# Performance work log

Measured on AMD Instinct MI355X. Metric: run time of the kernel, lower is better.

The kernel has to match this reference:

```python
import jax, jax.numpy as jnp
import numpy as np

N_NODES = 100000
N_EDGES = 1600000
D_IN = 128
D_HID = 128
GARMENT_SIZE = 80000


def setup_inputs() -> dict:
    key = jax.random.key(0)
    k1, k2, k3, k4, k5, k6 = jax.random.split(key, 6)
    notes = jax.random.normal(k1, (N_NODES, D_IN), dtype=jnp.float32)
    w = jax.random.normal(k2, (D_IN, D_HID), dtype=jnp.float32) * 0.05
    b = jax.random.normal(k3, (D_HID,), dtype=jnp.float32) * 0.05
    edge_src = jax.random.randint(k4, (N_EDGES,), 0, N_NODES, dtype=jnp.int32)
    edge_dst = jax.random.randint(k5, (N_EDGES,), 0, N_NODES, dtype=jnp.int32)
    edge_w = jax.random.uniform(k6, (N_EDGES,), dtype=jnp.float32)
    return {
        "notes": notes,
        "w": w,
        "b": b,
        "edge_src": edge_src,
        "edge_dst": edge_dst,
        "edge_w": edge_w,
        "garment_size": GARMENT_SIZE,
    }


def reference(notes, w, b, edge_src, edge_dst, edge_w, garment_size):
    # Dense projection: X0 = notes @ w   -> [N, H]
    X0 = jnp.einsum("nd,dh->nh", notes, w)
    # edge_convolution_template(edge_function=lambda x, y: y, reduction='weighted'):
    # X1[i] = sum over edges (i -> j) of a_ij * X0[j]
    msgs = X0[edge_dst] * edge_w[:, None]                      # [E, H] gather + scale
    X1 = jax.ops.segment_sum(msgs, edge_src, num_segments=notes.shape[0])  # [N, H]
    X = X1 + b
    # concat(act(X), X0[garment_size:]) along node axis -> [2N - garment_size, H]
    return jnp.concatenate([jax.nn.relu(X), X0[garment_size:]], axis=0)
```

## Files before the change

### kernel.cpp

```cpp
#include <hip/hip_runtime.h>

#define H 128
#define NPB 256
#define NB_MAX 1024
#define FILL_CH 4096
#define CNT_BLOCKS 256

static __device__ __forceinline__ unsigned short f2bf(float f) {
  unsigned u = __float_as_uint(f);
  u += 0x7FFFu + ((u >> 16) & 1u);
  return (unsigned short)(u >> 16);
}

__global__ __launch_bounds__(256) void gemm_count_kernel(
    const float* __restrict__ notes, const float* __restrict__ w,
    const int* __restrict__ g_ptr, const int* __restrict__ esrc,
    unsigned short* __restrict__ x0h, float* __restrict__ out,
    int* __restrict__ bucketCount, int nb, int n_nodes, int n_edges,
    int cntBlocks) {
  __shared__ float wtile[32 * H];
  __shared__ float ntile[64 * 32];
  const int tid = threadIdx.x;

  if (blockIdx.x < cntBlocks) {
    int* cnt = (int*)wtile;
    for (int i = tid; i < nb; i += 256) cnt[i] = 0;
    __syncthreads();
    int i = blockIdx.x * 256 + tid;
    const int stride = cntBlocks * 256;
    for (; i < n_edges; i += stride) atomicAdd(&cnt[esrc[i] >> 8], 1);
    __syncthreads();
    for (int j = tid; j < nb; j += 256) {
      const int c = cnt[j];
      if (c) atomicAdd(&bucketCount[j], c);
    }
    return;
  }

  const int tx = tid & 31;
  const int ty = tid >> 5;
  const int rowBlk = (blockIdx.x - cntBlocks) * 64;
  const int g = *g_ptr;

  float acc[8][4];
#pragma unroll
  for (int i = 0; i < 8; ++i)
#pragma unroll
    for (int j = 0; j < 4; ++j) acc[i][j] = 0.f;

  for (int kc = 0; kc < H; kc += 32) {
    __syncthreads();
    {
      const float4* wg = (const float4*)(w + (size_t)kc * H);
      float4* wl = (float4*)wtile;
#pragma unroll
      for (int i = 0; i < 4; ++i) wl[tid + i * 256] = wg[tid + i * 256];
    }
    {
      float4* nl = (float4*)ntile;
#pragma unroll
      for (int i = 0; i < 2; ++i) {
        const int idx = tid + i * 256;
        const int row = idx >> 3;
        const int q = idx & 7;
        const int rr = min(rowBlk + row, n_nodes - 1);
        nl[idx] = *(const float4*)(notes + (size_t)rr * H + kc + q * 4);
      }
    }
    __syncthreads();
#pragma unroll 8
    for (int kk = 0; kk < 32; ++kk) {
      const float4 b4 = *(const float4*)&wtile[kk * H + tx * 4];
      float a[8];
#pragma unroll
      for (int i = 0; i < 8; ++i) a[i] = ntile[(ty * 8 + i) * 32 + kk];
#pragma unroll
      for (int i = 0; i < 8; ++i) {
        acc[i][0] += a[i] * b4.x;
        acc[i][1] += a[i] * b4.y;
        acc[i][2] += a[i] * b4.z;
        acc[i][3] += a[i] * b4.w;
      }
    }
  }

#pragma unroll
  for (int i = 0; i < 8; ++i) {
    const int r = rowBlk + ty * 8 + i;
    if (r < n_nodes) {
      ushort4 h;
      h.x = f2bf(acc[i][0]);
      h.y = f2bf(acc[i][1]);
      h.z = f2bf(acc[i][2]);
      h.w = f2bf(acc[i][3]);
      *(ushort4*)(x0h + (size_t)r * H + tx * 4) = h;
      if (r >= g) {
        float4 v;
        v.x = acc[i][0]; v.y = acc[i][1]; v.z = acc[i][2]; v.w = acc[i][3];
        *(float4*)(out + (size_t)(n_nodes + r - g) * H + tx * 4) = v;
      }
    }
  }
}

__global__ __launch_bounds__(256) void bucket_scan_kernel(
    const int* __restrict__ bucketCount, int* __restrict__ bucketBase,
    int* __restrict__ bucketCursor, int* __restrict__ off, int nb,
    int n_nodes, int n_edges) {
  __shared__ int part[256];
  const int t = threadIdx.x;
  const int K = (nb + 255) / 256;
  const int lo = t * K;
  const int hi = min(lo + K, nb);
  int sum = 0;
  for (int i = lo; i < hi; ++i) sum += bucketCount[i];
  part[t] = sum;
  __syncthreads();
  for (int o = 1; o < 256; o <<= 1) {
    const int tv = (t >= o) ? part[t - o] : 0;
    __syncthreads();
    part[t] += tv;
    __syncthreads();
  }
  int run = (t == 0) ? 0 : part[t - 1];
  for (int i = lo; i < hi; ++i) {
    bucketBase[i] = run;
    bucketCursor[i] = run;
    run += bucketCount[i];
  }
  if (t == 255) {
    bucketBase[nb] = part[255];
    off[n_nodes] = n_edges;
  }
}

__global__ __launch_bounds__(256) void bucket_fill_kernel(
    const int* __restrict__ esrc, const int* __restrict__ edst,
    const float* __restrict__ ew, int* __restrict__ bucketCursor,
    int2* __restrict__ sedge, unsigned char* __restrict__ srcloc, int n_edges,
    int nb) {
  __shared__ int2 stage[FILL_CH];
  __shared__ unsigned short bkt16[FILL_CH];
  __shared__ unsigned char loc8[FILL_CH];
  __shared__ int cntA[NB_MAX];
  __shared__ int lbase[NB_MAX];
  __shared__ int cntC[NB_MAX];
  const int t = threadIdx.x;
  const int base = blockIdx.x * FILL_CH;
  const int edgesInBlock = min(FILL_CH, n_edges - base);

  for (int i = t; i < nb; i += 256) {
    cntA[i] = 0;
    cntC[i] = 0;
  }
  __syncthreads();

  int sreg[FILL_CH / 256];
#pragma unroll
  for (int k = 0; k < FILL_CH / 256; ++k) {
    const int e = base + k * 256 + t;
    if (e < n_edges) {
      const int s = esrc[e];
      sreg[k] = s;
      atomicAdd(&cntA[s >> 8], 1);
    }
  }
  __syncthreads();

  {
    __shared__ int part[256];
    const int K = (nb + 255) / 256;
    const int lo = t * K;
    const int hi = min(lo + K, nb);
    int sum = 0;
    for (int i = lo; i < hi; ++i) sum += cntA[i];
    part[t] = sum;
    __syncthreads();
    for (int o = 1; o < 256; o <<= 1) {
      const int tv = (t >= o) ? part[t - o] : 0;
      __syncthreads();
      part[t] += tv;
      __syncthreads();
    }
    int run = (t == 0) ? 0 : part[t - 1];
    for (int i = lo; i < hi; ++i) {
      lbase[i] = run;
      run += cntA[i];
    }
  }
  __syncthreads();
  for (int i = t; i < nb; i += 256) {
    const int c = cntA[i];
    cntA[i] = c ? atomicAdd(&bucketCursor[i], c) : 0;
  }
  __syncthreads();

#pragma unroll
  for (int k = 0; k < FILL_CH / 256; ++k) {
    const int e = base + k * 256 + t;
    if (e < n_edges) {
      const int s = sreg[k];
      const int b = s >> 8;
      const int r = atomicAdd(&cntC[b], 1);
      const int sp = lbase[b] + r;
      int2 pk;
      pk.x = edst[e];
      pk.y = __float_as_int(ew[e]);
      stage[sp] = pk;
      bkt16[sp] = (unsigned short)b;
      loc8[sp] = (unsigned char)(s & 255);
    }
  }
  __syncthreads();

  for (int j = t; j < edgesInBlock; j += 256) {
    const int b = bkt16[j];
    const int pos = cntA[b] + (j - lbase[b]);
    sedge[pos] = stage[j];
    srcloc[pos] = loc8[j];
  }
}

__global__ __launch_bounds__(256) void bucket_sort_kernel(
    const int* __restrict__ bucketBase, const int2* __restrict__ sedge,
    const unsigned char* __restrict__ srcloc, int2* __restrict__ sedge2,
    int* __restrict__ off, int n_nodes) {
  __shared__ int cnt[NPB];
  __shared__ int nodeOff[NPB];
  const int t = threadIdx.x;
  const int beg = bucketBase[blockIdx.x];
  const int end = bucketBase[blockIdx.x + 1];
  const int nodeBase = blockIdx.x * NPB;
  const int nodesInBucket = min(NPB, n_nodes - nodeBase);

  cnt[t] = 0;
  __syncthreads();
  for (int j = beg + t; j < end; j += 256) atomicAdd(&cnt[srcloc[j]], 1);
  __syncthreads();
  {
    const int v = cnt[t];
    nodeOff[t] = v;
    __syncthreads();
    for (int o = 1; o < 256; o <<= 1) {
      const int tv = (t >= o) ? nodeOff[t - o] : 0;
      __syncthreads();
      nodeOff[t] += tv;
      __syncthreads();
    }
    nodeOff[t] -= v;
  }
  if (t < nodesInBucket) off[nodeBase + t] = beg + nodeOff[t];
  cnt[t] = 0;
  __syncthreads();
  for (int j = beg + t; j < end; j += 256) {
    const int loc = srcloc[j];
    const int r = atomicAdd(&cnt[loc], 1);
    sedge2[beg + nodeOff[loc] + r] = sedge[j];
  }
}

__global__ __launch_bounds__(256) void gather_kernel(
    const int* __restrict__ off, const int2* __restrict__ sedge,
    const unsigned short* __restrict__ x0h, const float* __restrict__ b,
    float* __restrict__ out, int n_nodes) {
  const int wave = blockIdx.x * (blockDim.x >> 6) + (threadIdx.x >> 6);
  const int lane = threadIdx.x & 63;
  const int q = lane >> 4;
  const int l16 = lane & 15;
  const int node = wave * 4 + q;
  const bool valid = (node < n_nodes);

  int begH = 0, endH = 0;
  if (valid) {
    begH = off[node];
    endH = off[node + 1];
  }
  const int degH = endH - begH;
  const int dO = __shfl_xor(degH, 16);
  int kmin = min(degH, dO);
  int kmax = max(degH, dO);
  kmin = min(kmin, __shfl_xor(kmin, 32));
  kmax = max(kmax, __shfl_xor(kmax, 32));
  const int kfull = kmin & ~3;
  const int lastH = max(endH - 1, 0);
  const int2* __restrict__ sp = sedge + begH;

  const unsigned* __restrict__ x0u = (const unsigned*)x0h;

  float4 aLo[4], aHi[4];
#pragma unroll
  for (int j = 0; j < 4; ++j) {
    aLo[j] = make_float4(0.f, 0.f, 0.f, 0.f);
    aHi[j] = make_float4(0.f, 0.f, 0.f, 0.f);
  }

  int k = 0;
  for (; k < kfull; k += 4) {
    int2 m[4];
#pragma unroll
    for (int j = 0; j < 4; ++j) m[j] = sp[k + j];
    uint4 u[4];
#pragma unroll
    for (int j = 0; j < 4; ++j)
      u[j] = *(const uint4*)(x0u + (size_t)m[j].x * 64 + l16 * 4);
#pragma unroll
    for (int j = 0; j < 4; ++j) {
      const float wv = __int_as_float(m[j].y);
      aLo[j].x += __uint_as_float(u[j].x << 16) * wv;
      aLo[j].y += __uint_as_float(u[j].x & 0xFFFF0000u) * wv;
      aLo[j].z += __uint_as_float(u[j].y << 16) * wv;
      aLo[j].w += __uint_as_float(u[j].y & 0xFFFF0000u) * wv;
      aHi[j].x += __uint_as_float(u[j].z << 16) * wv;
      aHi[j].y += __uint_as_float(u[j].z & 0xFFFF0000u) * wv;
      aHi[j].z += __uint_as_float(u[j].w << 16) * wv;
      aHi[j].w += __uint_as_float(u[j].w & 0xFFFF0000u) * wv;
    }
  }
  for (; k < kmax; k += 4) {
    int2 m[4];
#pragma unroll
    for (int j = 0; j < 4; ++j) m[j] = sedge[min(begH + k + j, lastH)];
    uint4 u[4];
#pragma unroll
    for (int j = 0; j < 4; ++j)
      u[j] = *(const uint4*)(x0u + (size_t)m[j].x * 64 + l16 * 4);
#pragma unroll
    for (int j = 0; j < 4; ++j) {
      const float wv = (k + j < degH) ? __int_as_float(m[j].y) : 0.f;
      aLo[j].x += __uint_as_float(u[j].x << 16) * wv;
      aLo[j].y += __uint_as_float(u[j].x & 0xFFFF0000u) * wv;
      aLo[j].z += __uint_as_float(u[j].y << 16) * wv;
      aLo[j].w += __uint_as_float(u[j].y & 0xFFFF0000u) * wv;
      aHi[j].x += __uint_as_float(u[j].z << 16) * wv;
      aHi[j].y += __uint_as_float(u[j].z & 0xFFFF0000u) * wv;
      aHi[j].z += __uint_as_float(u[j].w << 16) * wv;
      aHi[j].w += __uint_as_float(u[j].w & 0xFFFF0000u) * wv;
    }
  }

  const float4 b0 = ((const float4*)b)[l16 * 2];
  const float4 b1 = ((const float4*)b)[l16 * 2 + 1];
  float4 r0, r1;
  r0.x = fmaxf(aLo[0].x + aLo[1].x + aLo[2].x + aLo[3].x + b0.x, 0.f);
  r0.y = fmaxf(aLo[0].y + aLo[1].y + aLo[2].y + aLo[3].y + b0.y, 0.f);
  r0.z = fmaxf(aLo[0].z + aLo[1].z + aLo[2].z + aLo[3].z + b0.z, 0.f);
  r0.w = fmaxf(aLo[0].w + aLo[1].w + aLo[2].w + aLo[3].w + b0.w, 0.f);
  r1.x = fmaxf(aHi[0].x + aHi[1].x + aHi[2].x + aHi[3].x + b1.x, 0.f);
  r1.y = fmaxf(aHi[0].y + aHi[1].y + aHi[2].y + aHi[3].y + b1.y, 0.f);
  r1.z = fmaxf(aHi[0].z + aHi[1].z + aHi[2].z + aHi[3].z + b1.z, 0.f);
  r1.w = fmaxf(aHi[0].w + aHi[1].w + aHi[2].w + aHi[3].w + b1.w, 0.f);
  if (valid) {
    float4* o4 = (float4*)out + (size_t)node * 32 + l16 * 2;
    o4[0] = r0;
    o4[1] = r1;
  }
}

__global__ __launch_bounds__(256) void scatter_kernel(
    const int* __restrict__ esrc, const int* __restrict__ edst,
    const float* __restrict__ ew, const unsigned short* __restrict__ x0h,
    float* __restrict__ acc, int n_edges) {
  const int lane = threadIdx.x & 63;
  const int waveId = blockIdx.x * (blockDim.x >> 6) + (threadIdx.x >> 6);
  const int nWaves = gridDim.x * (blockDim.x >> 6);
  const unsigned* __restrict__ x0u = (const unsigned*)x0h;
  for (int e = waveId; e < n_edges; e += nWaves) {
    const int s = esrc[e];
    const int d = edst[e];
    const float wt = ew[e];
    const unsigned u = x0u[(size_t)d * 64 + lane];
    float* p = acc + (size_t)s * H + lane * 2;
    atomicAdd(p, __uint_as_float(u << 16) * wt);
    atomicAdd(p + 1, __uint_as_float(u & 0xFFFF0000u) * wt);
  }
}

__global__ __launch_bounds__(256) void epilogue_kernel(
    float* __restrict__ out, const float* __restrict__ b, int n4) {
  const int i = blockIdx.x * blockDim.x + threadIdx.x;
  if (i >= n4) return;
  float4* o4 = (float4*)out;
  const float4* b4 = (const float4*)b;
  float4 v = o4[i];
  const float4 bb = b4[i & 31];
  v.x = fmaxf(v.x + bb.x, 0.f);
  v.y = fmaxf(v.y + bb.y, 0.f);
  v.z = fmaxf(v.z + bb.z, 0.f);
  v.w = fmaxf(v.w + bb.w, 0.f);
  o4[i] = v;
}

extern "C" void kernel_launch(void* const* d_in, const int* in_sizes, int n_in,
                              void* d_out, int out_size, void* d_ws, size_t ws_size,
                              hipStream_t stream) {
  const float* notes = (const float*)d_in[0];
  const float* w     = (const float*)d_in[1];
  const float* b     = (const float*)d_in[2];
  const int*   esrc  = (const int*)d_in[3];
  const int*   edst  = (const int*)d_in[4];
  const float* ew    = (const float*)d_in[5];
  const int*   gptr  = (const int*)d_in[6];

  const int n_nodes = in_sizes[0] / H;
  const int n_edges = in_sizes[3];
  float* out = (float*)d_out;

  const int nb = (n_nodes + NPB - 1) / NPB;

  char* ws = (char*)d_ws;
  size_t p = 0;
  auto alloc = [&](size_t bytes) -> char* {
    char* cur = ws + p;
    p = (p + bytes + 255) & ~(size_t)255;
    return cur;
  };
  unsigned short* x0h = (unsigned short*)alloc((size_t)n_nodes * H * 2);
  int*  bucketCount  = (int*)alloc((size_t)nb * sizeof(int));
  int*  bucketBase   = (int*)alloc(((size_t)nb + 1) * sizeof(int));
  int*  bucketCursor = (int*)alloc((size_t)nb * sizeof(int));
  int*  off          = (int*)alloc(((size_t)n_nodes + 1) * sizeof(int));
  int2* sedge        = (int2*)alloc((size_t)n_edges * sizeof(int2));
  int2* sedge2       = (int2*)alloc((size_t)n_edges * sizeof(int2));
  unsigned char* srcloc = (unsigned char*)alloc((size_t)n_edges);
  const bool ok = (p <= ws_size) && (nb <= NB_MAX);

  const int gemmBlocks = (n_nodes + 63) / 64;

  if (ok) {
    hipMemsetAsync(bucketCount, 0, (size_t)nb * sizeof(int), stream);
    gemm_count_kernel<<<gemmBlocks + CNT_BLOCKS, 256, 0, stream>>>(
        notes, w, gptr, esrc, x0h, out, bucketCount, nb, n_nodes, n_edges,
        CNT_BLOCKS);
    bucket_scan_kernel<<<1, 256, 0, stream>>>(bucketCount, bucketBase,
                                              bucketCursor, off, nb, n_nodes,
                                              n_edges);
    bucket_fill_kernel<<<(n_edges + FILL_CH - 1) / FILL_CH, 256, 0, stream>>>(
        esrc, edst, ew, bucketCursor, sedge, srcloc, n_edges, nb);
    bucket_sort_kernel<<<nb, 256, 0, stream>>>(bucketBase, sedge, srcloc,
                                               sedge2, off, n_nodes);
    const int waves = (n_nodes + 3) / 4;
    gather_kernel<<<(waves + 3) / 4, 256, 0, stream>>>(off, sedge2, x0h, b,
                                                       out, n_nodes);
  } else {
    gemm_count_kernel<<<gemmBlocks, 256, 0, stream>>>(
        notes, w, gptr, esrc, x0h, out, bucketCount, 0, n_nodes, n_edges, 0);
    hipMemsetAsync(d_out, 0, (size_t)n_nodes * H * sizeof(float), stream);
    scatter_kernel<<<2048, 256, 0, stream>>>(esrc, edst, ew, x0h, out, n_edges);
    const int n4 = n_nodes * H / 4;
    epilogue_kernel<<<(n4 + 255) / 256, 256, 0, stream>>>(out, b, n4);
  }
}
```

Baseline: 271.3 us.

## Fuse per-bucket node sort with gather into one LDS-staged kernel

The second-level bucket sort and the gather are merged into one kernel. Each block now sorts its bucket's edges by source node into shared memory and then immediately runs the weighted gather for its 128 nodes, so the sorted edge array and the per-node offset array no longer make a round trip through global memory. Bucket size is halved to 128 nodes so a bucket's edges (about 2048 on average) fit in a 4096-entry LDS buffer, with a chunked fallback that accumulates partial sums in the output. The cost is fewer, heavier blocks (about 782) with many barriers, and the gather now runs at block rather than wave granularity, which may lower occupancy and parallelism.

```diff
diff --git a/kernel.cpp b/kernel.cpp
--- a/kernel.cpp
+++ b/kernel.cpp
@@ -1,10 +1,11 @@
 #include <hip/hip_runtime.h>
 
 #define H 128
-#define NPB 256
+#define NPB 128
 #define NB_MAX 1024
 #define FILL_CH 4096
 #define CNT_BLOCKS 256
+#define GCAP 4096
 
 static __device__ __forceinline__ unsigned short f2bf(float f) {
   unsigned u = __float_as_uint(f);
@@ -28,7 +29,7 @@
     __syncthreads();
     int i = blockIdx.x * 256 + tid;
     const int stride = cntBlocks * 256;
-    for (; i < n_edges; i += stride) atomicAdd(&cnt[esrc[i] >> 8], 1);
+    for (; i < n_edges; i += stride) atomicAdd(&cnt[esrc[i] >> 7], 1);
     __syncthreads();
     for (int j = tid; j < nb; j += 256) {
       const int c = cnt[j];
@@ -105,8 +106,7 @@
 
 __global__ __launch_bounds__(256) void bucket_scan_kernel(
     const int* __restrict__ bucketCount, int* __restrict__ bucketBase,
-    int* __restrict__ bucketCursor, int* __restrict__ off, int nb,
-    int n_nodes, int n_edges) {
+    int* __restrict__ bucketCursor, int nb) {
   __shared__ int part[256];
   const int t = threadIdx.x;
   const int K = (nb + 255) / 256;
@@ -128,10 +128,7 @@
     bucketCursor[i] = run;
     run += bucketCount[i];
   }
-  if (t == 255) {
-    bucketBase[nb] = part[255];
-    off[n_nodes] = n_edges;
-  }
+  if (t == 255) bucketBase[nb] = part[255];
 }
 
 __global__ __launch_bounds__(256) void bucket_fill_kernel(
@@ -162,7 +159,7 @@
     if (e < n_edges) {
       const int s = esrc[e];
       sreg[k] = s;
-      atomicAdd(&cntA[s >> 8], 1);
+      atomicAdd(&cntA[s >> 7], 1);
     }
   }
   __syncthreads();
@@ -200,7 +197,7 @@
     const int e = base + k * 256 + t;
     if (e < n_edges) {
       const int s = sreg[k];
-      const int b = s >> 8;
+      const int b = s >> 7;
       const int r = atomicAdd(&cntC[b], 1);
       const int sp = lbase[b] + r;
       int2 pk;
@@ -208,7 +205,7 @@
       pk.y = __float_as_int(ew[e]);
       stage[sp] = pk;
       bkt16[sp] = (unsigned short)b;
-      loc8[sp] = (unsigned char)(s & 255);
+      loc8[sp] = (unsigned char)(s & 127);
     }
   }
   __syncthreads();
@@ -221,138 +218,151 @@
   }
 }
 
-__global__ __launch_bounds__(256) void bucket_sort_kernel(
+__global__ __launch_bounds__(256) void sortgather_kernel(
     const int* __restrict__ bucketBase, const int2* __restrict__ sedge,
-    const unsigned char* __restrict__ srcloc, int2* __restrict__ sedge2,
-    int* __restrict__ off, int n_nodes) {
+    const unsigned char* __restrict__ srcloc,
+    const unsigned short* __restrict__ x0h, const float* __restrict__ b,
+    float* __restrict__ out, int n_nodes) {
+  __shared__ int2 ledge[GCAP];
   __shared__ int cnt[NPB];
   __shared__ int nodeOff[NPB];
   const int t = threadIdx.x;
+  const int lane = t & 63;
+  const int wv = t >> 6;
+  const int q = lane >> 4;
+  const int l16 = lane & 15;
   const int beg = bucketBase[blockIdx.x];
   const int end = bucketBase[blockIdx.x + 1];
   const int nodeBase = blockIdx.x * NPB;
-  const int nodesInBucket = min(NPB, n_nodes - nodeBase);
-
-  cnt[t] = 0;
-  __syncthreads();
-  for (int j = beg + t; j < end; j += 256) atomicAdd(&cnt[srcloc[j]], 1);
-  __syncthreads();
-  {
-    const int v = cnt[t];
-    nodeOff[t] = v;
-    __syncthreads();
-    for (int o = 1; o < 256; o <<= 1) {
-      const int tv = (t >= o) ? nodeOff[t - o] : 0;
-      __syncthreads();
-      nodeOff[t] += tv;
-      __syncthreads();
-    }
-    nodeOff[t] -= v;
-  }
-  if (t < nodesInBucket) off[nodeBase + t] = beg + nodeOff[t];
-  cnt[t] = 0;
-  __syncthreads();
-  for (int j = beg + t; j < end; j += 256) {
-    const int loc = srcloc[j];
-    const int r = atomicAdd(&cnt[loc], 1);
-    sedge2[beg + nodeOff[loc] + r] = sedge[j];
-  }
-}
-
-__global__ __launch_bounds__(256) void gather_kernel(
-    const int* __restrict__ off, const int2* __restrict__ sedge,
-    const unsigned short* __restrict__ x0h, const float* __restrict__ b,
-    float* __restrict__ out, int n_nodes) {
-  const int wave = blockIdx.x * (blockDim.x >> 6) + (threadIdx.x >> 6);
-  const int lane = threadIdx.x & 63;
-  const int q = lane >> 4;
-  const int l16 = lane & 15;
-  const int node = wave * 4 + q;
-  const bool valid = (node < n_nodes);
-
-  int begH = 0, endH = 0;
-  if (valid) {
-    begH = off[node];
-    endH = off[node + 1];
-  }
-  const int degH = endH - begH;
-  const int dO = __shfl_xor(degH, 16);
-  int kmin = min(degH, dO);
-  int kmax = max(degH, dO);
-  kmin = min(kmin, __shfl_xor(kmin, 32));
-  kmax = max(kmax, __shfl_xor(kmax, 32));
-  const int kfull = kmin & ~3;
-  const int lastH = max(endH - 1, 0);
-  const int2* __restrict__ sp = sedge + begH;
-
   const unsigned* __restrict__ x0u = (const unsigned*)x0h;
-
-  float4 aLo[4], aHi[4];
-#pragma unroll
-  for (int j = 0; j < 4; ++j) {
-    aLo[j] = make_float4(0.f, 0.f, 0.f, 0.f);
-    aHi[j] = make_float4(0.f, 0.f, 0.f, 0.f);
-  }
-
-  int k = 0;
-  for (; k < kfull; k += 4) {
-    int2 m[4];
-#pragma unroll
-    for (int j = 0; j < 4; ++j) m[j] = sp[k + j];
-    uint4 u[4];
-#pragma unroll
-    for (int j = 0; j < 4; ++j)
-      u[j] = *(const uint4*)(x0u + (size_t)m[j].x * 64 + l16 * 4);
-#pragma unroll
-    for (int j = 0; j < 4; ++j) {
-      const float wv = __int_as_float(m[j].y);
-      aLo[j].x += __uint_as_float(u[j].x << 16) * wv;
-      aLo[j].y += __uint_as_float(u[j].x & 0xFFFF0000u) * wv;
-      aLo[j].z += __uint_as_float(u[j].y << 16) * wv;
-      aLo[j].w += __uint_as_float(u[j].y & 0xFFFF0000u) * wv;
-      aHi[j].x += __uint_as_float(u[j].z << 16) * wv;
-      aHi[j].y += __uint_as_float(u[j].z & 0xFFFF0000u) * wv;
-      aHi[j].z += __uint_as_float(u[j].w << 16) * wv;
-      aHi[j].w += __uint_as_float(u[j].w & 0xFFFF0000u) * wv;
-    }
-  }
-  for (; k < kmax; k += 4) {
-    int2 m[4];
-#pragma unroll
-    for (int j = 0; j < 4; ++j) m[j] = sedge[min(begH + k + j, lastH)];
-    uint4 u[4];
-#pragma unroll
-    for (int j = 0; j < 4; ++j)
-      u[j] = *(const uint4*)(x0u + (size_t)m[j].x * 64 + l16 * 4);
-#pragma unroll
-    for (int j = 0; j < 4; ++j) {
-      const float wv = (k + j < degH) ? __int_as_float(m[j].y) : 0.f;
-      aLo[j].x += __uint_as_float(u[j].x << 16) * wv;
-      aLo[j].y += __uint_as_float(u[j].x & 0xFFFF0000u) * wv;
-      aLo[j].z += __uint_as_float(u[j].y << 16) * wv;
-      aLo[j].w += __uint_as_float(u[j].y & 0xFFFF0000u) * wv;
-      aHi[j].x += __uint_as_float(u[j].z << 16) * wv;
-      aHi[j].y += __uint_as_float(u[j].z & 0xFFFF0000u) * wv;
-      aHi[j].z += __uint_as_float(u[j].w << 16) * wv;
-      aHi[j].w += __uint_as_float(u[j].w & 0xFFFF0000u) * wv;
-    }
-  }
+  const bool multi = (end - beg) > GCAP;
 
   const float4 b0 = ((const float4*)b)[l16 * 2];
   const float4 b1 = ((const float4*)b)[l16 * 2 + 1];
-  float4 r0, r1;
-  r0.x = fmaxf(aLo[0].x + aLo[1].x + aLo[2].x + aLo[3].x + b0.x, 0.f);
-  r0.y = fmaxf(aLo[0].y + aLo[1].y + aLo[2].y + aLo[3].y + b0.y, 0.f);
-  r0.z = fmaxf(aLo[0].z + aLo[1].z + aLo[2].z + aLo[3].z + b0.z, 0.f);
-  r0.w = fmaxf(aLo[0].w + aLo[1].w + aLo[2].w + aLo[3].w + b0.w, 0.f);
-  r1.x = fmaxf(aHi[0].x + aHi[1].x + aHi[2].x + aHi[3].x + b1.x, 0.f);
-  r1.y = fmaxf(aHi[0].y + aHi[1].y + aHi[2].y + aHi[3].y + b1.y, 0.f);
-  r1.z = fmaxf(aHi[0].z + aHi[1].z + aHi[2].z + aHi[3].z + b1.z, 0.f);
-  r1.w = fmaxf(aHi[0].w + aHi[1].w + aHi[2].w + aHi[3].w + b1.w, 0.f);
-  if (valid) {
-    float4* o4 = (float4*)out + (size_t)node * 32 + l16 * 2;
-    o4[0] = r0;
-    o4[1] = r1;
+
+  int chunkBeg = beg;
+  while (true) {
+    const int ccnt = min(end - chunkBeg, GCAP);
+    if (t < NPB) cnt[t] = 0;
+    __syncthreads();
+    for (int j = t; j < ccnt; j += 256)
+      atomicAdd(&cnt[srcloc[chunkBeg + j]], 1);
+    __syncthreads();
+    if (t < NPB) nodeOff[t] = cnt[t];
+    __syncthreads();
+    for (int o = 1; o < NPB; o <<= 1) {
+      int tv = 0;
+      if (t < NPB && t >= o) tv = nodeOff[t - o];
+      __syncthreads();
+      if (t < NPB) nodeOff[t] += tv;
+      __syncthreads();
+    }
+    if (t < NPB) {
+      nodeOff[t] -= cnt[t];
+      cnt[t] = 0;
+    }
+    __syncthreads();
+    for (int j = t; j < ccnt; j += 256) {
+      const int loc = srcloc[chunkBeg + j];
+      const int r = atomicAdd(&cnt[loc], 1);
+      ledge[nodeOff[loc] + r] = sedge[chunkBeg + j];
+    }
+    __syncthreads();
+    for (int rnd = 0; rnd < NPB / 16; ++rnd) {
+      const int loc = wv * (NPB / 4) + rnd * 4 + q;
+      const int node = nodeBase + loc;
+      const int o0 = nodeOff[loc];
+      const int o1 = (loc == NPB - 1) ? ccnt : nodeOff[loc + 1];
+      const int deg = o1 - o0;
+      int dmax = deg;
+      dmax = max(dmax, __shfl_xor(dmax, 16));
+      dmax = max(dmax, __shfl_xor(dmax, 32));
+      const int lastI = max(o1 - 1, 0);
+      float4 aLo[4], aHi[4];
+#pragma unroll
+      for (int j = 0; j < 4; ++j) {
+        aLo[j] = make_float4(0.f, 0.f, 0.f, 0.f);
+        aHi[j] = make_float4(0.f, 0.f, 0.f, 0.f);
+      }
+      for (int k = 0; k < dmax; k += 4) {
+        int2 m[4];
+#pragma unroll
+        for (int j = 0; j < 4; ++j) m[j] = ledge[min(o0 + k + j, lastI)];
+        uint4 u[4];
+#pragma unroll
+        for (int j = 0; j < 4; ++j)
+          u[j] = *(const uint4*)(x0u + (size_t)m[j].x * 64 + l16 * 4);
+#pragma unroll
+        for (int j = 0; j < 4; ++j) {
+          const float wf = (k + j < deg) ? __int_as_float(m[j].y) : 0.f;
+          aLo[j].x += __uint_as_float(u[j].x << 16) * wf;
+          aLo[j].y += __uint_as_float(u[j].x & 0xFFFF0000u) * wf;
+          aLo[j].z += __uint_as_float(u[j].y << 16) * wf;
+          aLo[j].w += __uint_as_float(u[j].y & 0xFFFF0000u) * wf;
+          aHi[j].x += __uint_as_float(u[j].z << 16) * wf;
+          aHi[j].y += __uint_as_float(u[j].z & 0xFFFF0000u) * wf;
+          aHi[j].z += __uint_as_float(u[j].w << 16) * wf;
+          aHi[j].w += __uint_as_float(u[j].w & 0xFFFF0000u) * wf;
+        }
+      }
+      if (node < n_nodes) {
+        float4 s0, s1;
+        s0.x = aLo[0].x + aLo[1].x + aLo[2].x + aLo[3].x;
+        s0.y = aLo[0].y + aLo[1].y + aLo[2].y + aLo[3].y;
+        s0.z = aLo[0].z + aLo[1].z + aLo[2].z + aLo[3].z;
+        s0.w = aLo[0].w + aLo[1].w + aLo[2].w + aLo[3].w;
+        s1.x = aHi[0].x + aHi[1].x + aHi[2].x + aHi[3].x;
+        s1.y = aHi[0].y + aHi[1].y + aHi[2].y + aHi[3].y;
+        s1.z = aHi[0].z + aHi[1].z + aHi[2].z + aHi[3].z;
+        s1.w = aHi[0].w + aHi[1].w + aHi[2].w + aHi[3].w;
+        float4* o4 = (float4*)out + (size_t)node * 32 + l16 * 2;
+        if (!multi) {
+          s0.x = fmaxf(s0.x + b0.x, 0.f);
+          s0.y = fmaxf(s0.y + b0.y, 0.f);
+          s0.z = fmaxf(s0.z + b0.z, 0.f);
+          s0.w = fmaxf(s0.w + b0.w, 0.f);
+          s1.x = fmaxf(s1.x + b1.x, 0.f);
+          s1.y = fmaxf(s1.y + b1.y, 0.f);
+          s1.z = fmaxf(s1.z + b1.z, 0.f);
+          s1.w = fmaxf(s1.w + b1.w, 0.f);
+          o4[0] = s0;
+          o4[1] = s1;
+        } else if (chunkBeg == beg) {
+          o4[0] = s0;
+          o4[1] = s1;
+        } else {
+          float4 p0 = o4[0], p1 = o4[1];
+          p0.x += s0.x; p0.y += s0.y; p0.z += s0.z; p0.w += s0.w;
+          p1.x += s1.x; p1.y += s1.y; p1.z += s1.z; p1.w += s1.w;
+          o4[0] = p0;
+          o4[1] = p1;
+        }
+      }
+    }
+    chunkBeg += GCAP;
+    if (chunkBeg >= end) break;
+    __syncthreads();
+  }
+
+  if (multi) {
+    for (int rnd = 0; rnd < NPB / 16; ++rnd) {
+      const int loc = wv * (NPB / 4) + rnd * 4 + q;
+      const int node = nodeBase + loc;
+      if (node < n_nodes) {
+        float4* o4 = (float4*)out + (size_t)node * 32 + l16 * 2;
+        float4 v0 = o4[0], v1 = o4[1];
+        v0.x = fmaxf(v0.x + b0.x, 0.f);
+        v0.y = fmaxf(v0.y + b0.y, 0.f);
+        v0.z = fmaxf(v0.z + b0.z, 0.f);
+        v0.w = fmaxf(v0.w + b0.w, 0.f);
+        v1.x = fmaxf(v1.x + b1.x, 0.f);
+        v1.y = fmaxf(v1.y + b1.y, 0.f);
+        v1.z = fmaxf(v1.z + b1.z, 0.f);
+        v1.w = fmaxf(v1.w + b1.w, 0.f);
+        o4[0] = v0;
+        o4[1] = v1;
+      }
+    }
   }
 }
 
@@ -418,9 +428,7 @@
   int*  bucketCount  = (int*)alloc((size_t)nb * sizeof(int));
   int*  bucketBase   = (int*)alloc(((size_t)nb + 1) * sizeof(int));
   int*  bucketCursor = (int*)alloc((size_t)nb * sizeof(int));
-  int*  off          = (int*)alloc(((size_t)n_nodes + 1) * sizeof(int));
   int2* sedge        = (int2*)alloc((size_t)n_edges * sizeof(int2));
-  int2* sedge2       = (int2*)alloc((size_t)n_edges * sizeof(int2));
   unsigned char* srcloc = (unsigned char*)alloc((size_t)n_edges);
   const bool ok = (p <= ws_size) && (nb <= NB_MAX);
 
@@ -432,15 +440,11 @@
         notes, w, gptr, esrc, x0h, out, bucketCount, nb, n_nodes, n_edges,
         CNT_BLOCKS);
     bucket_scan_kernel<<<1, 256, 0, stream>>>(bucketCount, bucketBase,
-                                              bucketCursor, off, nb, n_nodes,
-                                              n_edges);
+                                              bucketCursor, nb);
     bucket_fill_kernel<<<(n_edges + FILL_CH - 1) / FILL_CH, 256, 0, stream>>>(
         esrc, edst, ew, bucketCursor, sedge, srcloc, n_edges, nb);
-    bucket_sort_kernel<<<nb, 256, 0, stream>>>(bucketBase, sedge, srcloc,
-                                               sedge2, off, n_nodes);
-    const int waves = (n_nodes + 3) / 4;
-    gather_kernel<<<(waves + 3) / 4, 256, 0, stream>>>(off, sedge2, x0h, b,
-                                                       out, n_nodes);
+    sortgather_kernel<<<nb, 256, 0, stream>>>(bucketBase, sedge, srcloc, x0h,
+                                              b, out, n_nodes);
   } else {
     gemm_count_kernel<<<gemmBlocks, 256, 0, stream>>>(
         notes, w, gptr, esrc, x0h, out, bucketCount, 0, n_nodes, n_edges, 0);
```

After: 261.6 us. -3.6%, faster.
